# Kernel optimization log

Measured on AMD Instinct MI355X. Metric: run time of the kernel, lower is better.

The kernel has to match this reference:

```python
import jax, jax.numpy as jnp
import numpy as np

HEADS = 8
IN_C = 256
MDL = 512
N = 4
L = 4096
NE = 65536  # avg degree 16


def setup_inputs() -> dict:
    key = jax.random.key(0)
    ks = jax.random.split(key, 14)
    f32 = jnp.float32
    s = 0.05
    return {
        "queries": jax.random.normal(ks[0], (N, L, IN_C), f32),
        "keys": jax.random.normal(ks[1], (N, L, IN_C), f32),
        "values": jax.random.normal(ks[2], (N, L, IN_C), f32),
        "adj": jax.random.randint(ks[3], (2, NE), 0, L, dtype=jnp.int32),
        "edge_pos_enc": jax.random.normal(ks[4], (N, HEADS, NE), f32),
        "Wq": jax.random.normal(ks[5], (IN_C, MDL), f32) * s,
        "bq": jnp.zeros((MDL,), f32),
        "Wk": jax.random.normal(ks[6], (IN_C, MDL), f32) * s,
        "bk": jnp.zeros((MDL,), f32),
        "Wv": jax.random.normal(ks[7], (IN_C, MDL), f32) * s,
        "bv": jnp.zeros((MDL,), f32),
        "Wo": jax.random.normal(ks[8], (MDL, MDL), f32) * s,
        "bo": jnp.zeros((MDL,), f32),
    }


def reference(queries, keys, values, adj, edge_pos_enc, Wq, bq, Wk, bk, Wv, bv, Wo, bo):
    n, l, _ = queries.shape
    h = HEADS
    e = MDL // h  # per-head dim
    temp = 1.0 / jnp.sqrt(jnp.asarray(e, queries.dtype))
    dst, src = adj[0], adj[1]

    def split(x):  # (n, l, mdl) -> (n*h, l, e)
        return x.reshape(n, l, h, e).transpose(0, 2, 1, 3).reshape(n * h, l, e)

    q = split(queries @ Wq + bq)
    k = split(keys @ Wk + bk)
    v = split(values @ Wv + bv)
    epe = edge_pos_enc.reshape(n * h, NE)

    def head(qh, kh, vh, eh):
        # qh,kh,vh: (l, e); eh: (Ne,)
        scores = temp * (jnp.sum(qh[dst] * kh[src], axis=-1) + eh)  # (Ne,)
        m = jax.ops.segment_max(scores, dst, num_segments=l)
        p = jnp.exp(scores - m[dst])
        z = jax.ops.segment_sum(p, dst, num_segments=l)
        alpha = p / z[dst]  # segment softmax keyed by dst (adj[0])
        return jax.ops.segment_sum(alpha[:, None] * vh[src], dst, num_segments=l)  # (l, e)

    out = jax.vmap(head)(q, k, v, epe)  # (n*h, l, e)
    out = out.reshape(n, h, l, e).transpose(0, 2, 1, 3).reshape(n, l, h * e)
    return out @ Wo + bo
```

## Files before the change

### kernel.cpp

```cpp
#include <hip/hip_runtime.h>
#include <hip/hip_bf16.h>
#include <math.h>
#include <stdint.h>

#define HEADS 8
#define IN_C  256
#define MDL   512
#define NB    4
#define LL    4096
#define NE    65536
#define EDIM  64
#define TEMP  0.125f

typedef __bf16 bf16x8 __attribute__((ext_vector_type(8)));
typedef float  f32x4  __attribute__((ext_vector_type(4)));
typedef short  short8 __attribute__((ext_vector_type(8)));

__device__ __forceinline__ void glds16(const void* g, void* l) {
    __builtin_amdgcn_global_load_lds(
        (const __attribute__((address_space(1))) void*)g,
        (__attribute__((address_space(3))) void*)l, 16, 0, 0);
}

__device__ __forceinline__ short8 cvt8(float4 a, float4 b) {
    union { short8 v; __hip_bfloat16 h[8]; } u;
    u.h[0] = __float2bfloat16(a.x); u.h[1] = __float2bfloat16(a.y);
    u.h[2] = __float2bfloat16(a.z); u.h[3] = __float2bfloat16(a.w);
    u.h[4] = __float2bfloat16(b.x); u.h[5] = __float2bfloat16(b.y);
    u.h[6] = __float2bfloat16(b.z); u.h[7] = __float2bfloat16(b.w);
    return u.v;
}

__global__ __launch_bounds__(256) void gemm_qkv(
    const float* __restrict__ A0, const float* __restrict__ A1,
    const float* __restrict__ A2,
    const __hip_bfloat16* __restrict__ B0, const __hip_bfloat16* __restrict__ B1,
    const __hip_bfloat16* __restrict__ B2,
    const float* __restrict__ b0, const float* __restrict__ b1,
    const float* __restrict__ b2,
    __hip_bfloat16* __restrict__ C0, __hip_bfloat16* __restrict__ C1,
    __hip_bfloat16* __restrict__ C2, int M, int N, int K)
{
    __shared__ __align__(16) __hip_bfloat16 As[128 * 32];
    __shared__ __align__(16) __hip_bfloat16 Bs[128 * 32];

    const int z = blockIdx.z;
    const float* A           = (z == 0) ? A0 : (z == 1) ? A1 : A2;
    const __hip_bfloat16* Bt = (z == 0) ? B0 : (z == 1) ? B1 : B2;
    const float* bias        = (z == 0) ? b0 : (z == 1) ? b1 : b2;
    __hip_bfloat16* C        = (z == 0) ? C0 : (z == 1) ? C1 : C2;

    const int tid  = threadIdx.x;
    const int lane = tid & 63;
    const int w    = tid >> 6;
    const int wr   = w >> 1, wc = w & 1;
    const int bm   = blockIdx.y * 128, bn = blockIdx.x * 128;

    const int r0  = tid >> 2;
    const int cc0 = tid & 3;
    const int ca0 = cc0 ^ (r0 & 3);
    const int r1  = r0 + 64;
    const int ca1 = cc0 ^ (r1 & 3);
    const float* gA0 = A + (size_t)(bm + r0) * K + ca0 * 8;
    const float* gA1 = A + (size_t)(bm + r1) * K + ca1 * 8;
    __hip_bfloat16* lA0w = As + r0 * 32 + cc0 * 8;
    __hip_bfloat16* lA1w = As + r1 * 32 + cc0 * 8;

    const int cb0 = (tid & 3) ^ (r0 & 3);
    const int cb1 = (tid & 3) ^ (r1 & 3);
    const __hip_bfloat16* gB0 = Bt + (size_t)(bn + r0) * K + cb0 * 8;
    const __hip_bfloat16* gB1 = Bt + (size_t)(bn + r1) * K + cb1 * 8;
    __hip_bfloat16* lB0 = Bs + (size_t)(w * 64) * 8;
    __hip_bfloat16* lB1 = Bs + (size_t)(256 + w * 64) * 8;

    int fa[4], fb[4];
    #pragma unroll
    for (int i = 0; i < 4; i++) {
        int rA = wr * 64 + i * 16 + (lane & 15);
        fa[i] = rA * 32 + (((lane >> 4) ^ (rA & 3)) * 8);
        int rB = wc * 64 + i * 16 + (lane & 15);
        fb[i] = rB * 32 + (((lane >> 4) ^ (rB & 3)) * 8);
    }

    f32x4 acc[4][4] = {};

    for (int k0 = 0; k0 < K; k0 += 32) {
        glds16(gB0 + k0, lB0);
        glds16(gB1 + k0, lB1);
        float4 a0  = *(const float4*)(gA0 + k0);
        float4 a0b = *(const float4*)(gA0 + k0 + 4);
        float4 a1  = *(const float4*)(gA1 + k0);
        float4 a1b = *(const float4*)(gA1 + k0 + 4);
        *(short8*)lA0w = cvt8(a0, a0b);
        *(short8*)lA1w = cvt8(a1, a1b);
        __syncthreads();

        bf16x8 av[4], bv[4];
        #pragma unroll
        for (int i = 0; i < 4; i++) av[i] = *(const bf16x8*)(As + fa[i]);
        #pragma unroll
        for (int i = 0; i < 4; i++) bv[i] = *(const bf16x8*)(Bs + fb[i]);
        #pragma unroll
        for (int mi = 0; mi < 4; mi++)
            #pragma unroll
            for (int ni = 0; ni < 4; ni++)
                acc[mi][ni] = __builtin_amdgcn_mfma_f32_16x16x32_bf16(
                    av[mi], bv[ni], acc[mi][ni], 0, 0, 0);
        __syncthreads();
    }

    #pragma unroll
    for (int mi = 0; mi < 4; mi++) {
        int row = bm + wr * 64 + mi * 16 + (lane >> 4) * 4;
        #pragma unroll
        for (int ni = 0; ni < 4; ni++) {
            int col = bn + wc * 64 + ni * 16 + (lane & 15);
            float bb = bias[col];
            #pragma unroll
            for (int j = 0; j < 4; j++)
                C[(size_t)(row + j) * N + col] = __float2bfloat16(acc[mi][ni][j] + bb);
        }
    }
}

__global__ __launch_bounds__(256) void gemm_out(
    const __hip_bfloat16* __restrict__ A, const __hip_bfloat16* __restrict__ Bt,
    const float* __restrict__ bias, float* __restrict__ C, int M, int N, int K)
{
    __shared__ __align__(16) __hip_bfloat16 As[128 * 64];
    __shared__ __align__(16) __hip_bfloat16 Bs[128 * 64];

    const int tid  = threadIdx.x;
    const int lane = tid & 63;
    const int w    = tid >> 6;
    const int wr   = w >> 1, wc = w & 1;
    const int bm   = blockIdx.y * 128, bn = blockIdx.x * 128;

    const __hip_bfloat16* gA[4];
    const __hip_bfloat16* gB[4];
    __hip_bfloat16* lA[4];
    __hip_bfloat16* lB[4];
    #pragma unroll
    for (int it = 0; it < 4; it++) {
        int idx = it * 256 + tid;
        int r = idx >> 3;
        int c = (idx & 7) ^ (r & 7);
        gA[it] = A  + (size_t)(bm + r) * K + c * 8;
        gB[it] = Bt + (size_t)(bn + r) * K + c * 8;
        lA[it] = As + (size_t)(it * 256 + w * 64) * 8;
        lB[it] = Bs + (size_t)(it * 256 + w * 64) * 8;
    }

    int fa[2][4], fb[2][4];
    #pragma unroll
    for (int kk = 0; kk < 2; kk++)
        #pragma unroll
        for (int i = 0; i < 4; i++) {
            int rA = wr * 64 + i * 16 + (lane & 15);
            int gc = kk * 4 + (lane >> 4);
            fa[kk][i] = rA * 64 + (gc ^ (rA & 7)) * 8;
            int rB = wc * 64 + i * 16 + (lane & 15);
            fb[kk][i] = rB * 64 + (gc ^ (rB & 7)) * 8;
        }

    f32x4 acc[4][4] = {};

    for (int k0 = 0; k0 < K; k0 += 64) {
        #pragma unroll
        for (int it = 0; it < 4; it++) {
            glds16(gA[it] + k0, lA[it]);
            glds16(gB[it] + k0, lB[it]);
        }
        __syncthreads();

        #pragma unroll
        for (int kk = 0; kk < 2; kk++) {
            bf16x8 av[4], bv[4];
            #pragma unroll
            for (int i = 0; i < 4; i++) av[i] = *(const bf16x8*)(As + fa[kk][i]);
            #pragma unroll
            for (int i = 0; i < 4; i++) bv[i] = *(const bf16x8*)(Bs + fb[kk][i]);
            #pragma unroll
            for (int mi = 0; mi < 4; mi++)
                #pragma unroll
                for (int ni = 0; ni < 4; ni++)
                    acc[mi][ni] = __builtin_amdgcn_mfma_f32_16x16x32_bf16(
                        av[mi], bv[ni], acc[mi][ni], 0, 0, 0);
        }
        __syncthreads();
    }

    #pragma unroll
    for (int mi = 0; mi < 4; mi++) {
        int row = bm + wr * 64 + mi * 16 + (lane >> 4) * 4;
        #pragma unroll
        for (int ni = 0; ni < 4; ni++) {
            int col = bn + wc * 64 + ni * 16 + (lane & 15);
            float bb = bias[col];
            #pragma unroll
            for (int j = 0; j < 4; j++)
                C[(size_t)(row + j) * N + col] = acc[mi][ni][j] + bb;
        }
    }
}

__global__ void count_edges(const int* __restrict__ dst, int* __restrict__ counts, int ne) {
    int e = blockIdx.x * blockDim.x + threadIdx.x;
    if (e < ne) atomicAdd(&counts[dst[e]], 1);
}

__global__ __launch_bounds__(1024) void scan_offsets(
    const int* __restrict__ counts, int* __restrict__ offsets,
    int* __restrict__ cursor, int* __restrict__ reorder)
{
    __shared__ int wsum[16];
    __shared__ int bcnt[9], boff[9];
    const int tid  = threadIdx.x;
    const int lane = tid & 63;
    const int wid  = tid >> 6;

    if (tid < 9) bcnt[tid] = 0;

    int c[4];
    int base = tid * 4;
    int s = 0;
    #pragma unroll
    for (int i = 0; i < 4; i++) { c[i] = counts[base + i]; s += c[i]; }

    int v = s;
    #pragma unroll
    for (int off = 1; off < 64; off <<= 1) {
        int t = __shfl_up(v, off);
        if (lane >= off) v += t;
    }
    if (lane == 63) wsum[wid] = v;
    __syncthreads();
    if (wid == 0) {
        int wv = (lane < 16) ? wsum[lane] : 0;
        #pragma unroll
        for (int off = 1; off < 16; off <<= 1) {
            int t = __shfl_up(wv, off);
            if (lane >= off) wv += t;
        }
        if (lane < 16) wsum[lane] = wv;
    }
    __syncthreads();

    int prefix = (wid > 0 ? wsum[wid - 1] : 0) + (v - s);
    int run = prefix;
    int mybk[4];
    #pragma unroll
    for (int i = 0; i < 4; i++) {
        offsets[base + i] = run;
        cursor[base + i]  = run;
        run += c[i];
        int sc = (c[i] + 7) >> 3; if (sc > 8) sc = 8;
        mybk[i] = 8 - sc;
        atomicAdd(&bcnt[mybk[i]], 1);
    }
    if (tid == 1023) offsets[4096] = run;
    __syncthreads();
    if (tid == 0) {
        int acc0 = 0;
        #pragma unroll
        for (int b = 0; b < 9; b++) { boff[b] = acc0; acc0 += bcnt[b]; }
    }
    __syncthreads();
    #pragma unroll
    for (int i = 0; i < 4; i++) {
        int pos = atomicAdd(&boff[mybk[i]], 1);
        reorder[pos] = base + i;
    }
}

__global__ __launch_bounds__(256) void prep(
    const int* __restrict__ dst, const int* __restrict__ srcarr,
    const float* __restrict__ epe, int* __restrict__ cursor,
    int* __restrict__ src_s, float* __restrict__ epe_s,
    const float* __restrict__ Wq, const float* __restrict__ Wk,
    const float* __restrict__ Wv, const float* __restrict__ Wo,
    __hip_bfloat16* __restrict__ Wqt, __hip_bfloat16* __restrict__ Wkt,
    __hip_bfloat16* __restrict__ Wvt, __hip_bfloat16* __restrict__ Wot)
{
    __shared__ float t[32][33];
    const int b = blockIdx.x;

    if (b < 256) {
        int e = b * 256 + threadIdx.x;
        int p = atomicAdd(&cursor[dst[e]], 1);
        src_s[p] = srcarr[e];
        #pragma unroll
        for (int n = 0; n < NB; n++) {
            float4 a2, b2;
            const float* base = epe + (size_t)(n * HEADS) * NE + e;
            a2.x = base[0 * NE]; a2.y = base[1 * NE]; a2.z = base[2 * NE]; a2.w = base[3 * NE];
            b2.x = base[4 * NE]; b2.y = base[5 * NE]; b2.z = base[6 * NE]; b2.w = base[7 * NE];
            float* o = epe_s + ((size_t)n * NE + p) * 8;
            *(float4*)o       = a2;
            *(float4*)(o + 4) = b2;
        }
    } else {
        int bb = b - 256;
        const float* W; __hip_bfloat16* Wt; int K, tt;
        if (bb < 384) {
            int m = bb >> 7; tt = bb & 127; K = IN_C;
            W  = (m == 0) ? Wq  : (m == 1) ? Wk  : Wv;
            Wt = (m == 0) ? Wqt : (m == 1) ? Wkt : Wvt;
        } else {
            tt = bb - 384; K = MDL; W = Wo; Wt = Wot;
        }
        const int N = MDL;
        int bx = (tt & 15) * 32;
        int by = (tt >> 4) * 32;
        int tx = threadIdx.x & 31, ty = threadIdx.x >> 5;
        #pragma unroll
        for (int i = 0; i < 4; i++)
            t[ty + i * 8][tx] = W[(size_t)(by + ty + i * 8) * N + bx + tx];
        __syncthreads();
        #pragma unroll
        for (int i = 0; i < 4; i++)
            Wt[(size_t)(bx + ty + i * 8) * K + by + tx] =
                __float2bfloat16(t[tx][ty + i * 8]);
    }
}

__global__ __launch_bounds__(256) void sparse_attn7(
    const __hip_bfloat16* __restrict__ Qb, const __hip_bfloat16* __restrict__ Kb,
    const __hip_bfloat16* __restrict__ Vb,
    const int* __restrict__ src_s, const float* __restrict__ epe_s,
    const int* __restrict__ offsets, const int* __restrict__ reorder,
    __hip_bfloat16* __restrict__ O)
{
    const int lane = threadIdx.x & 63;
    const int wid  = threadIdx.x >> 6;
    const int bid  = blockIdx.x;
    const int xcd  = bid & 7;
    const int n    = xcd >> 1;
    const int base = ((bid >> 3) << 1) | (xcd & 1);
    const int dstn = reorder[(base << 2) | wid];
    const int task = n * LL + dstn;
    const int hg   = lane >> 3;

    const size_t rowbase = (size_t)task * MDL;
    const int beg = offsets[dstn];
    const int end = offsets[dstn + 1];
    const int deg = end - beg;

    union { short8 v8; __hip_bfloat16 h[8]; } uo;
    if (deg == 0) {
        #pragma unroll
        for (int j = 0; j < 8; j++) uo.h[j] = __float2bfloat16(0.0f);
        *(short8*)(O + rowbase + lane * 8) = uo.v8;
        return;
    }

    bf16x8 q8 = *(const bf16x8*)(Qb + rowbase + lane * 8);
    float qf[8];
    #pragma unroll
    for (int j = 0; j < 8; j++) qf[j] = (float)q8[j];

    const __hip_bfloat16* Kn = Kb + (size_t)n * LL * MDL + lane * 8;
    const __hip_bfloat16* Vn = Vb + (size_t)n * LL * MDL + lane * 8;
    const float* pe_n = epe_s + (size_t)n * NE * 8 + hg;

    float acc[8] = {};

    if (deg <= 64) {
        const int my_src = src_s[beg + ((lane < deg) ? lane : (deg - 1))];

        float m = -INFINITY, z = 0.0f;
        float s_st[8];

        #pragma unroll
        for (int slot = 0; slot < 8; slot++) {
            const int r0 = slot * 8;
            if (r0 < deg) {
                bf16x8 kk[8];
                #pragma unroll
                for (int j = 0; j < 8; j++) {
                    int s = __shfl(my_src, r0 + j);
                    kk[j] = *(const bf16x8*)(Kn + (size_t)s * MDL);
                }
                const int rel_mine = r0 + (lane & 7);
                float pp = (rel_mine < deg)
                         ? pe_n[(size_t)(beg + rel_mine) * 8] : -INFINITY;

                float p[8];
                #pragma unroll
                for (int j = 0; j < 8; j++) {
                    float d = 0.0f;
                    #pragma unroll
                    for (int dd = 0; dd < 8; dd++)
                        d = fmaf(qf[dd], (float)kk[j][dd], d);
                    p[j] = d;
                }
                float n0, n1, n2, n3, u0, u1, sraw;
                {
                    float a0 = (lane & 1) ? p[1] : p[0];
                    float b0 = (lane & 1) ? p[0] : p[1];
                    n0 = a0 + __shfl_xor(b0, 1);
                    float a1 = (lane & 1) ? p[3] : p[2];
                    float b1 = (lane & 1) ? p[2] : p[3];
                    n1 = a1 + __shfl_xor(b1, 1);
                    float a2 = (lane & 1) ? p[5] : p[4];
                    float b2 = (lane & 1) ? p[4] : p[5];
                    n2 = a2 + __shfl_xor(b2, 1);
                    float a3 = (lane & 1) ? p[7] : p[6];
                    float b3 = (lane & 1) ? p[6] : p[7];
                    n3 = a3 + __shfl_xor(b3, 1);

                    float c0 = (lane & 2) ? n1 : n0;
                    float d0 = (lane & 2) ? n0 : n1;
                    u0 = c0 + __shfl_xor(d0, 2);
                    float c1 = (lane & 2) ? n3 : n2;
                    float d1 = (lane & 2) ? n2 : n3;
                    u1 = c1 + __shfl_xor(d1, 2);

                    float e0 = (lane & 4) ? u1 : u0;
                    float f0 = (lane & 4) ? u0 : u1;
                    sraw = e0 + __shfl_xor(f0, 4);
                }

                float sc_my = TEMP * (sraw + pp);
                s_st[slot] = sc_my;

                float gm = sc_my;
                gm = fmaxf(gm, __shfl_xor(gm, 1));
                gm = fmaxf(gm, __shfl_xor(gm, 2));
                gm = fmaxf(gm, __shfl_xor(gm, 4));
                float mnew = fmaxf(m, gm);
                float e_my = __expf(sc_my - mnew);
                float gs = e_my;
                gs += __shfl_xor(gs, 1);
                gs += __shfl_xor(gs, 2);
                gs += __shfl_xor(gs, 4);
                z = z * __expf(m - mnew) + gs;
                m = mnew;
            } else {
                s_st[slot] = -INFINITY;
            }
        }

        const float zinv = 1.0f / z;
        float a_st[8];
        #pragma unroll
        for (int slot = 0; slot < 8; slot++)
            a_st[slot] = __expf(s_st[slot] - m) * zinv;

        #pragma unroll
        for (int slot = 0; slot < 8; slot++) {
            const int r0 = slot * 8;
            if (r0 < deg) {
                bf16x8 vv[8];
                #pragma unroll
                for (int j = 0; j < 8; j++) {
                    int s = __shfl(my_src, r0 + j);
                    vv[j] = *(const bf16x8*)(Vn + (size_t)s * MDL);
                }
                #pragma unroll
                for (int j = 0; j < 8; j++) {
                    float al = __shfl(a_st[slot], (lane & 56) | j);
                    #pragma unroll
                    for (int dd = 0; dd < 8; dd++)
                        acc[dd] = fmaf(al, (float)vv[j][dd], acc[dd]);
                }
            }
        }
    } else {
        float m = -INFINITY, z = 0.0f;
        bf16x8 ka[4], va[4], kb2[4], vb2[4];
        float  pa[4], pb2[4];

        #define LOADB(i, kk, vv, pp)                                        \
            _Pragma("unroll")                                               \
            for (int j = 0; j < 4; j++) {                                   \
                int idx = (i) + j;                                          \
                int ok  = idx < end;                                        \
                int s   = ok ? src_s[idx] : src_s[beg];                     \
                size_t rk = (size_t)s * MDL;                                \
                kk[j] = *(const bf16x8*)(Kn + rk);                          \
                vv[j] = *(const bf16x8*)(Vn + rk);                          \
                pp[j] = ok ? pe_n[(size_t)idx * 8] : -INFINITY;             \
            }

        #define COMPUTE(kk, vv, pp)                                         \
        {                                                                   \
            float sc4[4];                                                   \
            _Pragma("unroll")                                               \
            for (int j = 0; j < 4; j++) {                                   \
                float d = 0.0f;                                             \
                _Pragma("unroll")                                           \
                for (int dd = 0; dd < 8; dd++) d += qf[dd] * (float)kk[j][dd]; \
                d += __shfl_xor(d, 1);                                      \
                d += __shfl_xor(d, 2);                                      \
                d += __shfl_xor(d, 4);                                      \
                sc4[j] = TEMP * (d + pp[j]);                                \
            }                                                               \
            float mb   = fmaxf(fmaxf(sc4[0], sc4[1]), fmaxf(sc4[2], sc4[3])); \
            float mnew = fmaxf(m, mb);                                      \
            float sc   = __expf(m - mnew);                                  \
            float pe0 = __expf(sc4[0] - mnew);                              \
            float pe1 = __expf(sc4[1] - mnew);                              \
            float pe2 = __expf(sc4[2] - mnew);                              \
            float pe3 = __expf(sc4[3] - mnew);                              \
            z = z * sc + (pe0 + pe1 + pe2 + pe3);                           \
            _Pragma("unroll")                                               \
            for (int dd = 0; dd < 8; dd++) {                                \
                float tt = acc[dd] * sc;                                    \
                tt = fmaf(pe0, (float)vv[0][dd], tt);                       \
                tt = fmaf(pe1, (float)vv[1][dd], tt);                       \
                tt = fmaf(pe2, (float)vv[2][dd], tt);                       \
                tt = fmaf(pe3, (float)vv[3][dd], tt);                       \
                acc[dd] = tt;                                               \
            }                                                               \
            m = mnew;                                                       \
        }

        LOADB(beg, ka, va, pa)
        for (int i = beg; i < end; i += 4) {
            if (i + 4 < end) { LOADB(i + 4, kb2, vb2, pb2) }
            COMPUTE(ka, va, pa)
            #pragma unroll
            for (int j = 0; j < 4; j++) { ka[j] = kb2[j]; va[j] = vb2[j]; pa[j] = pb2[j]; }
        }
        float inv = 1.0f / z;
        #pragma unroll
        for (int dd = 0; dd < 8; dd++) acc[dd] *= inv;
        #undef LOADB
        #undef COMPUTE
    }

    #pragma unroll
    for (int j = 0; j < 8; j++) uo.h[j] = __float2bfloat16(acc[j]);
    *(short8*)(O + rowbase + lane * 8) = uo.v8;
}

extern "C" void kernel_launch(void* const* d_in, const int* in_sizes, int n_in,
                              void* d_out, int out_size, void* d_ws, size_t ws_size,
                              hipStream_t stream)
{
    const float* queries = (const float*)d_in[0];
    const float* keys    = (const float*)d_in[1];
    const float* values  = (const float*)d_in[2];
    const int*   adj     = (const int*)d_in[3];
    const float* epe     = (const float*)d_in[4];
    const float* Wq = (const float*)d_in[5];
    const float* bq = (const float*)d_in[6];
    const float* Wk = (const float*)d_in[7];
    const float* bk = (const float*)d_in[8];
    const float* Wv = (const float*)d_in[9];
    const float* bv = (const float*)d_in[10];
    const float* Wo = (const float*)d_in[11];
    const float* bo = (const float*)d_in[12];
    float* out = (float*)d_out;

    const int* dst = adj;
    const int* src = adj + NE;

    const int    M   = NB * LL;
    const size_t NLM = (size_t)M * MDL;

    char* w = (char*)d_ws;
    __hip_bfloat16* Qb  = (__hip_bfloat16*)w; w += NLM * 2;
    __hip_bfloat16* Kb  = (__hip_bfloat16*)w; w += NLM * 2;
    __hip_bfloat16* Vb  = (__hip_bfloat16*)w; w += NLM * 2;
    __hip_bfloat16* Ob  = (__hip_bfloat16*)w; w += NLM * 2;
    __hip_bfloat16* Wqt = (__hip_bfloat16*)w; w += (size_t)MDL * IN_C * 2;
    __hip_bfloat16* Wkt = (__hip_bfloat16*)w; w += (size_t)MDL * IN_C * 2;
    __hip_bfloat16* Wvt = (__hip_bfloat16*)w; w += (size_t)MDL * IN_C * 2;
    __hip_bfloat16* Wot = (__hip_bfloat16*)w; w += (size_t)MDL * MDL * 2;
    int* counts  = (int*)w; w += 4096 * sizeof(int);
    int* offsets = (int*)w; w += 4100 * sizeof(int);
    int* cursor  = (int*)w; w += 4096 * sizeof(int);
    int* reorder = (int*)w; w += 4096 * sizeof(int);
    int*   src_s = (int*)w; w += NE * sizeof(int);
    float* epe_s = (float*)w; w += (size_t)NB * NE * 8 * sizeof(float);

    hipMemsetAsync(counts, 0, 4096 * sizeof(int), stream);
    count_edges<<<NE / 256, 256, 0, stream>>>(dst, counts, NE);
    scan_offsets<<<1, 1024, 0, stream>>>(counts, offsets, cursor, reorder);

    prep<<<896, 256, 0, stream>>>(dst, src, epe, cursor, src_s, epe_s,
                                  Wq, Wk, Wv, Wo, Wqt, Wkt, Wvt, Wot);

    dim3 g3(MDL / 128, M / 128, 3);
    gemm_qkv<<<g3, 256, 0, stream>>>(queries, keys, values, Wqt, Wkt, Wvt,
                                     bq, bk, bv, Qb, Kb, Vb, M, MDL, IN_C);

    sparse_attn7<<<(NB * LL) / 4, 256, 0, stream>>>(Qb, Kb, Vb, src_s, epe_s,
                                                    offsets, reorder, Ob);

    dim3 g(MDL / 128, M / 128);
    gemm_out<<<g, 256, 0, stream>>>(Ob, Wot, bo, out, M, MDL, MDL);
}
```

Before: 138.3 us.

## Split sparse attention into score and output passes; widen QKV GEMM K-tile

Result: faster. 132.0 us (-4.5%).

```diff
diff --git a/kernel.cpp b/kernel.cpp
--- a/kernel.cpp
+++ b/kernel.cpp
@@ -41,8 +41,8 @@
     __hip_bfloat16* __restrict__ C0, __hip_bfloat16* __restrict__ C1,
     __hip_bfloat16* __restrict__ C2, int M, int N, int K)
 {
-    __shared__ __align__(16) __hip_bfloat16 As[128 * 32];
-    __shared__ __align__(16) __hip_bfloat16 Bs[128 * 32];
+    __shared__ __align__(16) __hip_bfloat16 As[128 * 64];
+    __shared__ __align__(16) __hip_bfloat16 Bs[128 * 64];
 
     const int z = blockIdx.z;
     const float* A           = (z == 0) ? A0 : (z == 1) ? A1 : A2;
@@ -56,56 +56,61 @@
     const int wr   = w >> 1, wc = w & 1;
     const int bm   = blockIdx.y * 128, bn = blockIdx.x * 128;
 
-    const int r0  = tid >> 2;
-    const int cc0 = tid & 3;
-    const int ca0 = cc0 ^ (r0 & 3);
-    const int r1  = r0 + 64;
-    const int ca1 = cc0 ^ (r1 & 3);
-    const float* gA0 = A + (size_t)(bm + r0) * K + ca0 * 8;
-    const float* gA1 = A + (size_t)(bm + r1) * K + ca1 * 8;
-    __hip_bfloat16* lA0w = As + r0 * 32 + cc0 * 8;
-    __hip_bfloat16* lA1w = As + r1 * 32 + cc0 * 8;
-
-    const int cb0 = (tid & 3) ^ (r0 & 3);
-    const int cb1 = (tid & 3) ^ (r1 & 3);
-    const __hip_bfloat16* gB0 = Bt + (size_t)(bn + r0) * K + cb0 * 8;
-    const __hip_bfloat16* gB1 = Bt + (size_t)(bn + r1) * K + cb1 * 8;
-    __hip_bfloat16* lB0 = Bs + (size_t)(w * 64) * 8;
-    __hip_bfloat16* lB1 = Bs + (size_t)(256 + w * 64) * 8;
-
-    int fa[4], fb[4];
-    #pragma unroll
-    for (int i = 0; i < 4; i++) {
-        int rA = wr * 64 + i * 16 + (lane & 15);
-        fa[i] = rA * 32 + (((lane >> 4) ^ (rA & 3)) * 8);
-        int rB = wc * 64 + i * 16 + (lane & 15);
-        fb[i] = rB * 32 + (((lane >> 4) ^ (rB & 3)) * 8);
-    }
+    const float*          gA[4];
+    const __hip_bfloat16* gB[4];
+    __hip_bfloat16* lAw[4];
+    __hip_bfloat16* lB[4];
+    #pragma unroll
+    for (int it = 0; it < 4; it++) {
+        int idx  = it * 256 + tid;
+        int r    = idx >> 3;
+        int cpos = idx & 7;
+        int cdat = cpos ^ (r & 7);
+        gA[it]  = A  + (size_t)(bm + r) * K + cdat * 8;
+        gB[it]  = Bt + (size_t)(bn + r) * K + cdat * 8;
+        lAw[it] = As + r * 64 + cpos * 8;
+        lB[it]  = Bs + (size_t)(it * 256 + w * 64) * 8;
+    }
+
+    int fa[2][4], fb[2][4];
+    #pragma unroll
+    for (int kk = 0; kk < 2; kk++)
+        #pragma unroll
+        for (int i = 0; i < 4; i++) {
+            int rA = wr * 64 + i * 16 + (lane & 15);
+            int gc = kk * 4 + (lane >> 4);
+            fa[kk][i] = rA * 64 + (gc ^ (rA & 7)) * 8;
+            int rB = wc * 64 + i * 16 + (lane & 15);
+            fb[kk][i] = rB * 64 + (gc ^ (rB & 7)) * 8;
+        }
 
     f32x4 acc[4][4] = {};
 
-    for (int k0 = 0; k0 < K; k0 += 32) {
-        glds16(gB0 + k0, lB0);
-        glds16(gB1 + k0, lB1);
-        float4 a0  = *(const float4*)(gA0 + k0);
-        float4 a0b = *(const float4*)(gA0 + k0 + 4);
-        float4 a1  = *(const float4*)(gA1 + k0);
-        float4 a1b = *(const float4*)(gA1 + k0 + 4);
-        *(short8*)lA0w = cvt8(a0, a0b);
-        *(short8*)lA1w = cvt8(a1, a1b);
+    for (int k0 = 0; k0 < K; k0 += 64) {
+        #pragma unroll
+        for (int it = 0; it < 4; it++) glds16(gB[it] + k0, lB[it]);
+        #pragma unroll
+        for (int it = 0; it < 4; it++) {
+            float4 a = *(const float4*)(gA[it] + k0);
+            float4 b = *(const float4*)(gA[it] + k0 + 4);
+            *(short8*)lAw[it] = cvt8(a, b);
+        }
         __syncthreads();
 
-        bf16x8 av[4], bv[4];
-        #pragma unroll
-        for (int i = 0; i < 4; i++) av[i] = *(const bf16x8*)(As + fa[i]);
-        #pragma unroll
-        for (int i = 0; i < 4; i++) bv[i] = *(const bf16x8*)(Bs + fb[i]);
-        #pragma unroll
-        for (int mi = 0; mi < 4; mi++)
-            #pragma unroll
-            for (int ni = 0; ni < 4; ni++)
-                acc[mi][ni] = __builtin_amdgcn_mfma_f32_16x16x32_bf16(
-                    av[mi], bv[ni], acc[mi][ni], 0, 0, 0);
+        #pragma unroll
+        for (int kk = 0; kk < 2; kk++) {
+            bf16x8 av[4], bv[4];
+            #pragma unroll
+            for (int i = 0; i < 4; i++) av[i] = *(const bf16x8*)(As + fa[kk][i]);
+            #pragma unroll
+            for (int i = 0; i < 4; i++) bv[i] = *(const bf16x8*)(Bs + fb[kk][i]);
+            #pragma unroll
+            for (int mi = 0; mi < 4; mi++)
+                #pragma unroll
+                for (int ni = 0; ni < 4; ni++)
+                    acc[mi][ni] = __builtin_amdgcn_mfma_f32_16x16x32_bf16(
+                        av[mi], bv[ni], acc[mi][ni], 0, 0, 0);
+        }
         __syncthreads();
     }
 
@@ -324,12 +329,11 @@
     }
 }
 
-__global__ __launch_bounds__(256) void sparse_attn7(
+__global__ __launch_bounds__(256) void sparse_score(
     const __hip_bfloat16* __restrict__ Qb, const __hip_bfloat16* __restrict__ Kb,
-    const __hip_bfloat16* __restrict__ Vb,
     const int* __restrict__ src_s, const float* __restrict__ epe_s,
     const int* __restrict__ offsets, const int* __restrict__ reorder,
-    __hip_bfloat16* __restrict__ O)
+    float* __restrict__ score_s, float2* __restrict__ mz)
 {
     const int lane = threadIdx.x & 63;
     const int wid  = threadIdx.x >> 6;
@@ -341,35 +345,24 @@
     const int task = n * LL + dstn;
     const int hg   = lane >> 3;
 
-    const size_t rowbase = (size_t)task * MDL;
     const int beg = offsets[dstn];
     const int end = offsets[dstn + 1];
     const int deg = end - beg;
-
-    union { short8 v8; __hip_bfloat16 h[8]; } uo;
-    if (deg == 0) {
-        #pragma unroll
-        for (int j = 0; j < 8; j++) uo.h[j] = __float2bfloat16(0.0f);
-        *(short8*)(O + rowbase + lane * 8) = uo.v8;
-        return;
-    }
-
-    bf16x8 q8 = *(const bf16x8*)(Qb + rowbase + lane * 8);
+    if (deg == 0) return;
+
+    bf16x8 q8 = *(const bf16x8*)(Qb + (size_t)task * MDL + lane * 8);
     float qf[8];
     #pragma unroll
     for (int j = 0; j < 8; j++) qf[j] = (float)q8[j];
 
     const __hip_bfloat16* Kn = Kb + (size_t)n * LL * MDL + lane * 8;
-    const __hip_bfloat16* Vn = Vb + (size_t)n * LL * MDL + lane * 8;
     const float* pe_n = epe_s + (size_t)n * NE * 8 + hg;
-
-    float acc[8] = {};
+    float* sc_n = score_s + (size_t)n * NE * 8 + hg;
+
+    float m = -INFINITY, z = 0.0f;
 
     if (deg <= 64) {
         const int my_src = src_s[beg + ((lane < deg) ? lane : (deg - 1))];
-
-        float m = -INFINITY, z = 0.0f;
-        float s_st[8];
 
         #pragma unroll
         for (int slot = 0; slot < 8; slot++) {
@@ -422,7 +415,8 @@
                 }
 
                 float sc_my = TEMP * (sraw + pp);
-                s_st[slot] = sc_my;
+                if (rel_mine < deg)
+                    sc_n[(size_t)(beg + rel_mine) * 8] = sc_my;
 
                 float gm = sc_my;
                 gm = fmaxf(gm, __shfl_xor(gm, 1));
@@ -436,16 +430,85 @@
                 gs += __shfl_xor(gs, 4);
                 z = z * __expf(m - mnew) + gs;
                 m = mnew;
-            } else {
-                s_st[slot] = -INFINITY;
             }
         }
-
-        const float zinv = 1.0f / z;
-        float a_st[8];
-        #pragma unroll
-        for (int slot = 0; slot < 8; slot++)
-            a_st[slot] = __expf(s_st[slot] - m) * zinv;
+    } else {
+        for (int i = beg; i < end; i += 4) {
+            float sc4[4];
+            #pragma unroll
+            for (int j = 0; j < 4; j++) {
+                int idx = i + j;
+                int ok  = idx < end;
+                int s   = ok ? src_s[idx] : src_s[beg];
+                bf16x8 kk = *(const bf16x8*)(Kn + (size_t)s * MDL);
+                float pp = ok ? pe_n[(size_t)idx * 8] : -INFINITY;
+                float d = 0.0f;
+                #pragma unroll
+                for (int dd = 0; dd < 8; dd++) d += qf[dd] * (float)kk[dd];
+                d += __shfl_xor(d, 1);
+                d += __shfl_xor(d, 2);
+                d += __shfl_xor(d, 4);
+                sc4[j] = TEMP * (d + pp);
+                if (ok && (lane & 7) == 0)
+                    sc_n[(size_t)idx * 8] = sc4[j];
+            }
+            float mb   = fmaxf(fmaxf(sc4[0], sc4[1]), fmaxf(sc4[2], sc4[3]));
+            float mnew = fmaxf(m, mb);
+            float sc   = __expf(m - mnew);
+            float s0 = __expf(sc4[0] - mnew);
+            float s1 = __expf(sc4[1] - mnew);
+            float s2 = __expf(sc4[2] - mnew);
+            float s3 = __expf(sc4[3] - mnew);
+            z = z * sc + (s0 + s1 + s2 + s3);
+            m = mnew;
+        }
+    }
+
+    if ((lane & 7) == 0) {
+        float2 v; v.x = m; v.y = 1.0f / z;
+        mz[(size_t)task * 8 + hg] = v;
+    }
+}
+
+__global__ __launch_bounds__(256) void sparse_out(
+    const __hip_bfloat16* __restrict__ Vb,
+    const int* __restrict__ src_s, const float* __restrict__ score_s,
+    const int* __restrict__ offsets, const int* __restrict__ reorder,
+    const float2* __restrict__ mz, __hip_bfloat16* __restrict__ O)
+{
+    const int lane = threadIdx.x & 63;
+    const int wid  = threadIdx.x >> 6;
+    const int bid  = blockIdx.x;
+    const int xcd  = bid & 7;
+    const int n    = xcd >> 1;
+    const int base = ((bid >> 3) << 1) | (xcd & 1);
+    const int dstn = reorder[(base << 2) | wid];
+    const int task = n * LL + dstn;
+    const int hg   = lane >> 3;
+
+    const size_t rowbase = (size_t)task * MDL;
+    const int beg = offsets[dstn];
+    const int end = offsets[dstn + 1];
+    const int deg = end - beg;
+
+    union { short8 v8; __hip_bfloat16 h[8]; } uo;
+    if (deg == 0) {
+        #pragma unroll
+        for (int j = 0; j < 8; j++) uo.h[j] = __float2bfloat16(0.0f);
+        *(short8*)(O + rowbase + lane * 8) = uo.v8;
+        return;
+    }
+
+    float2 mzv = mz[(size_t)task * 8 + hg];
+    const float m = mzv.x, zinv = mzv.y;
+
+    const __hip_bfloat16* Vn = Vb + (size_t)n * LL * MDL + lane * 8;
+    const float* sc_n = score_s + (size_t)n * NE * 8 + hg;
+
+    float acc[8] = {};
+
+    if (deg <= 64) {
+        const int my_src = src_s[beg + ((lane < deg) ? lane : (deg - 1))];
 
         #pragma unroll
         for (int slot = 0; slot < 8; slot++) {
@@ -457,9 +520,13 @@
                     int s = __shfl(my_src, r0 + j);
                     vv[j] = *(const bf16x8*)(Vn + (size_t)s * MDL);
                 }
+                const int rel_mine = r0 + (lane & 7);
+                float sc = (rel_mine < deg)
+                         ? sc_n[(size_t)(beg + rel_mine) * 8] : -INFINITY;
+                float a_l = __expf(sc - m) * zinv;
                 #pragma unroll
                 for (int j = 0; j < 8; j++) {
-                    float al = __shfl(a_st[slot], (lane & 56) | j);
+                    float al = __shfl(a_l, (lane & 56) | j);
                     #pragma unroll
                     for (int dd = 0; dd < 8; dd++)
                         acc[dd] = fmaf(al, (float)vv[j][dd], acc[dd]);
@@ -467,67 +534,20 @@
             }
         }
     } else {
-        float m = -INFINITY, z = 0.0f;
-        bf16x8 ka[4], va[4], kb2[4], vb2[4];
-        float  pa[4], pb2[4];
-
-        #define LOADB(i, kk, vv, pp)                                        \
-            _Pragma("unroll")                                               \
-            for (int j = 0; j < 4; j++) {                                   \
-                int idx = (i) + j;                                          \
-                int ok  = idx < end;                                        \
-                int s   = ok ? src_s[idx] : src_s[beg];                     \
-                size_t rk = (size_t)s * MDL;                                \
-                kk[j] = *(const bf16x8*)(Kn + rk);                          \
-                vv[j] = *(const bf16x8*)(Vn + rk);                          \
-                pp[j] = ok ? pe_n[(size_t)idx * 8] : -INFINITY;             \
+        for (int i = beg; i < end; i += 4) {
+            #pragma unroll
+            for (int j = 0; j < 4; j++) {
+                int idx = i + j;
+                int ok  = idx < end;
+                int s   = ok ? src_s[idx] : src_s[beg];
+                bf16x8 vv = *(const bf16x8*)(Vn + (size_t)s * MDL);
+                float sc = ok ? sc_n[(size_t)idx * 8] : -INFINITY;
+                float al = __expf(sc - m) * zinv;
+                #pragma unroll
+                for (int dd = 0; dd < 8; dd++)
+                    acc[dd] = fmaf(al, (float)vv[dd], acc[dd]);
             }
-
-        #define COMPUTE(kk, vv, pp)                                         \
-        {                                                                   \
-            float sc4[4];                                                   \
-            _Pragma("unroll")                                               \
-            for (int j = 0; j < 4; j++) {                                   \
-                float d = 0.0f;                                             \
-                _Pragma("unroll")                                           \
-                for (int dd = 0; dd < 8; dd++) d += qf[dd] * (float)kk[j][dd]; \
-                d += __shfl_xor(d, 1);                                      \
-                d += __shfl_xor(d, 2);                                      \
-                d += __shfl_xor(d, 4);                                      \
-                sc4[j] = TEMP * (d + pp[j]);                                \
-            }                                                               \
-            float mb   = fmaxf(fmaxf(sc4[0], sc4[1]), fmaxf(sc4[2], sc4[3])); \
-            float mnew = fmaxf(m, mb);                                      \
-            float sc   = __expf(m - mnew);                                  \
-            float pe0 = __expf(sc4[0] - mnew);                              \
-            float pe1 = __expf(sc4[1] - mnew);                              \
-            float pe2 = __expf(sc4[2] - mnew);                              \
-            float pe3 = __expf(sc4[3] - mnew);                              \
-            z = z * sc + (pe0 + pe1 + pe2 + pe3);                           \
-            _Pragma("unroll")                                               \
-            for (int dd = 0; dd < 8; dd++) {                                \
-                float tt = acc[dd] * sc;                                    \
-                tt = fmaf(pe0, (float)vv[0][dd], tt);                       \
-                tt = fmaf(pe1, (float)vv[1][dd], tt);                       \
-                tt = fmaf(pe2, (float)vv[2][dd], tt);                       \
-                tt = fmaf(pe3, (float)vv[3][dd], tt);                       \
-                acc[dd] = tt;                                               \
-            }                                                               \
-            m = mnew;                                                       \
-        }
-
-        LOADB(beg, ka, va, pa)
-        for (int i = beg; i < end; i += 4) {
-            if (i + 4 < end) { LOADB(i + 4, kb2, vb2, pb2) }
-            COMPUTE(ka, va, pa)
-            #pragma unroll
-            for (int j = 0; j < 4; j++) { ka[j] = kb2[j]; va[j] = vb2[j]; pa[j] = pb2[j]; }
-        }
-        float inv = 1.0f / z;
-        #pragma unroll
-        for (int dd = 0; dd < 8; dd++) acc[dd] *= inv;
-        #undef LOADB
-        #undef COMPUTE
+        }
     }
 
     #pragma unroll
@@ -574,7 +594,9 @@
     int* cursor  = (int*)w; w += 4096 * sizeof(int);
     int* reorder = (int*)w; w += 4096 * sizeof(int);
     int*   src_s = (int*)w; w += NE * sizeof(int);
-    float* epe_s = (float*)w; w += (size_t)NB * NE * 8 * sizeof(float);
+    float* epe_s   = (float*)w;  w += (size_t)NB * NE * 8 * sizeof(float);
+    float* score_s = (float*)w;  w += (size_t)NB * NE * 8 * sizeof(float);
+    float2* mz     = (float2*)w; w += (size_t)M * 8 * sizeof(float2);
 
     hipMemsetAsync(counts, 0, 4096 * sizeof(int), stream);
     count_edges<<<NE / 256, 256, 0, stream>>>(dst, counts, NE);
@@ -587,8 +609,10 @@
     gemm_qkv<<<g3, 256, 0, stream>>>(queries, keys, values, Wqt, Wkt, Wvt,
                                      bq, bk, bv, Qb, Kb, Vb, M, MDL, IN_C);
 
-    sparse_attn7<<<(NB * LL) / 4, 256, 0, stream>>>(Qb, Kb, Vb, src_s, epe_s,
-                                                    offsets, reorder, Ob);
+    sparse_score<<<(NB * LL) / 4, 256, 0, stream>>>(Qb, Kb, src_s, epe_s,
+                                                    offsets, reorder, score_s, mz);
+    sparse_out<<<(NB * LL) / 4, 256, 0, stream>>>(Vb, src_s, score_s,
+                                                  offsets, reorder, mz, Ob);
 
     dim3 g(MDL / 128, M / 128);
     gemm_out<<<g, 256, 0, stream>>>(Ob, Wot, bo, out, M, MDL, MDL);
```
